# Optimization experiments

Hardware: AMD Instinct MI355X
Metric: run time of the kernel (lower is better)

## Reference

```python
import jax, jax.numpy as jnp
import numpy as np

B, T = 1, 128
R = 200000          # neurons * 4 receptor channels (output current dim)
LGN = 17400         # LGN source neurons
BKG = 100           # background source neurons
NNZ_L = 1_000_000   # lgn synapses
NNZ_B = 400_000     # bkg synapses


def setup_inputs() -> dict:
    key = jax.random.key(0)
    ks = jax.random.split(key, 8)
    lgn_spikes = (jax.random.uniform(ks[0], (B, T, LGN)) < 0.05).astype(jnp.float32)
    bkg_spikes = (jax.random.uniform(ks[1], (B, T, BKG)) < 0.1).astype(jnp.float32)
    lgn_rows = jnp.sort(jax.random.randint(ks[2], (NNZ_L,), 0, R, dtype=jnp.int32))
    lgn_cols = jax.random.randint(ks[3], (NNZ_L,), 0, LGN, dtype=jnp.int32)
    lgn_weights = jax.random.normal(ks[4], (NNZ_L,), dtype=jnp.float32) * 0.1
    bkg_rows = jnp.sort(jax.random.randint(ks[5], (NNZ_B,), 0, R, dtype=jnp.int32))
    bkg_cols = jax.random.randint(ks[6], (NNZ_B,), 0, BKG, dtype=jnp.int32)
    bkg_weights = jax.random.normal(ks[7], (NNZ_B,), dtype=jnp.float32) * 0.1
    return {
        "lgn_spikes": lgn_spikes, "bkg_spikes": bkg_spikes,
        "lgn_rows": lgn_rows, "lgn_cols": lgn_cols, "lgn_weights": lgn_weights,
        "bkg_rows": bkg_rows, "bkg_cols": bkg_cols, "bkg_weights": bkg_weights,
    }


def _sparse_current(spikes, rows, cols, weights, n_rows):
    # spikes: (B, T, C). Equivalent to transpose(sparse(R,C) @ spikes_2d^T)
    # reshaped back to (B, T, R).
    b, t, c = spikes.shape
    x2d = spikes.reshape(b * t, c)                       # (BT, C)
    vals = weights[:, None] * x2d[:, cols].T             # (nnz, BT) gathered contributions
    out = jax.ops.segment_sum(vals, rows, num_segments=n_rows)  # (R, BT)
    return out.T.reshape(b, t, n_rows)


def reference(lgn_spikes, bkg_spikes, lgn_rows, lgn_cols, lgn_weights,
              bkg_rows, bkg_cols, bkg_weights):
    lgn_current = _sparse_current(lgn_spikes, lgn_rows, lgn_cols, lgn_weights, R)
    bkg_current = _sparse_current(bkg_spikes, bkg_rows, bkg_cols, bkg_weights, R)
    return lgn_current + bkg_current
```

## Files before the change

kernel.cpp:

```cpp
#include <hip/hip_runtime.h>

#define T_STEPS 128

typedef float vfloat4 __attribute__((ext_vector_type(4)));

__global__ __launch_bounds__(256) void prep_kernel(
    const float* __restrict__ lgn_spikes, int lgn_C, uint2* __restrict__ lgn_mask,
    const float* __restrict__ bkg_spikes, int bkg_C, uint2* __restrict__ bkg_mask,
    const int* __restrict__ lgn_rows, int nnz_l, int* __restrict__ lgn_start,
    const int* __restrict__ bkg_rows, int nnz_b, int* __restrict__ bkg_start,
    int R)
{
    int gid = blockIdx.x * 256 + threadIdx.x;
    int totC = lgn_C + bkg_C;

    if (gid < totC) {
        const float* sp; uint2* mask; int C, cc;
        if (gid < lgn_C) { sp = lgn_spikes; mask = lgn_mask; C = lgn_C; cc = gid; }
        else             { sp = bkg_spikes; mask = bkg_mask; C = bkg_C; cc = gid - lgn_C; }
        unsigned int m0 = 0u, m1 = 0u, m2 = 0u, m3 = 0u;
        #pragma unroll 4
        for (int t = 0; t < 32; ++t) {
            if (sp[(size_t)(t)       * C + cc] != 0.0f) m0 |= (1u << t);
            if (sp[(size_t)(t +  32) * C + cc] != 0.0f) m1 |= (1u << t);
            if (sp[(size_t)(t +  64) * C + cc] != 0.0f) m2 |= (1u << t);
            if (sp[(size_t)(t +  96) * C + cc] != 0.0f) m3 |= (1u << t);
        }
        mask[(size_t)0 * C + cc] = make_uint2(m0, m1);
        mask[(size_t)1 * C + cc] = make_uint2(m2, m3);
        return;
    }

    int i = gid - totC;
    const int* rows; int nnz; int* start;
    if (i < nnz_l) { rows = lgn_rows; nnz = nnz_l; start = lgn_start; }
    else {
        i -= nnz_l;
        if (i >= nnz_b) return;
        rows = bkg_rows; nnz = nnz_b; start = bkg_start;
    }
    int cur  = rows[i];
    int prev = (i == 0) ? -1 : rows[i - 1];
    for (int rr = prev + 1; rr <= cur; ++rr) start[rr] = i;
    if (i == nnz - 1)
        for (int rr = cur + 1; rr <= R; ++rr) start[rr] = nnz;
}

__global__ __launch_bounds__(256, 4) void sparse_lut_kernel(
    const int* __restrict__ lgn_cols, const float* __restrict__ lgn_w,
    const int* __restrict__ lgn_start,
    const int* __restrict__ bkg_cols, const float* __restrict__ bkg_w,
    const int* __restrict__ bkg_start,
    const uint2* __restrict__ lgn_mask,
    const uint2* __restrict__ bkg_mask,
    int lgn_C, int bkg_C, int R,
    float* __restrict__ out)
{
    __shared__ float4 lut[16];
    __shared__ float tile[16 * 260];
    const int tid = threadIdx.x;
    if (tid < 16)
        lut[tid] = make_float4((float)(tid & 1), (float)((tid >> 1) & 1),
                               (float)((tid >> 2) & 1), (float)((tid >> 3) & 1));

    const int r0 = blockIdx.x * 256;
    const int r  = r0 + tid;
    const int q  = blockIdx.y;

    float acc[64];
    #pragma unroll
    for (int t = 0; t < 64; ++t) acc[t] = 0.0f;

    const uint2* lm = lgn_mask + (size_t)q * lgn_C;
    const uint2* bm = bkg_mask + (size_t)q * bkg_C;

    int l0 = 0, l1 = 0, g0 = 0, g1 = 0;
    if (r < R) {
        l0 = lgn_start[r]; l1 = lgn_start[r + 1];
        g0 = bkg_start[r]; g1 = bkg_start[r + 1];
    }
    __syncthreads();

    #define ACC_WORD(mw, base, wv)                                           \
        _Pragma("unroll")                                                    \
        for (int nb = 0; nb < 8; ++nb) {                                     \
            float4 s = lut[((mw) >> (nb * 4)) & 15u];                        \
            acc[(base) + nb * 4 + 0] = fmaf(wv, s.x, acc[(base) + nb * 4 + 0]); \
            acc[(base) + nb * 4 + 1] = fmaf(wv, s.y, acc[(base) + nb * 4 + 1]); \
            acc[(base) + nb * 4 + 2] = fmaf(wv, s.z, acc[(base) + nb * 4 + 2]); \
            acc[(base) + nb * 4 + 3] = fmaf(wv, s.w, acc[(base) + nb * 4 + 3]); \
        }

    #define ACC_RANGE(cols_a, w_a, mask_p, I0, I1)                           \
    {                                                                        \
        int i0 = (I0), i1 = (I1);                                            \
        if (i0 < i1) {                                                       \
            float w0 = w_a[i0];                                              \
            int   c1 = 0; float w1 = 0.0f;                                   \
            if (i0 + 1 < i1) { c1 = cols_a[i0 + 1]; w1 = w_a[i0 + 1]; }      \
            uint2 m0 = mask_p[cols_a[i0]];                                   \
            for (int i = i0; i < i1; ++i) {                                  \
                uint2 m1v = make_uint2(0u, 0u);                              \
                if (i + 1 < i1) m1v = mask_p[c1];                            \
                int c2 = 0; float w2 = 0.0f;                                 \
                if (i + 2 < i1) { c2 = cols_a[i + 2]; w2 = w_a[i + 2]; }     \
                ACC_WORD(m0.x, 0,  w0)                                       \
                ACC_WORD(m0.y, 32, w0)                                       \
                m0 = m1v; w0 = w1; c1 = c2; w1 = w2;                         \
            }                                                                \
        }                                                                    \
    }

    ACC_RANGE(lgn_cols, lgn_w, lm, l0, l1)
    ACC_RANGE(bkg_cols, bkg_w, bm, g0, g1)
    #undef ACC_RANGE
    #undef ACC_WORD

    const int wid  = tid >> 6;
    const int lane = tid & 63;
    #pragma unroll
    for (int pass = 0; pass < 4; ++pass) {
        #pragma unroll
        for (int p = 0; p < 16; ++p)
            tile[p * 260 + tid] = acc[pass * 16 + p];
        __syncthreads();
        #pragma unroll
        for (int pp = 0; pp < 4; ++pp) {
            int p  = wid * 4 + pp;
            int rr = r0 + 4 * lane;
            vfloat4 v = *(const vfloat4*)&tile[p * 260 + 4 * lane];
            int t = q * 64 + pass * 16 + p;
            float* dst = &out[(size_t)t * R + rr];
            if (rr + 3 < R) {
                __builtin_nontemporal_store(v, (vfloat4*)dst);
            } else {
                if (rr     < R) __builtin_nontemporal_store(v.x, dst);
                if (rr + 1 < R) __builtin_nontemporal_store(v.y, dst + 1);
                if (rr + 2 < R) __builtin_nontemporal_store(v.z, dst + 2);
            }
        }
        __syncthreads();
    }
}

__global__ __launch_bounds__(256) void sparse_fallback_kernel(
    const int* __restrict__ lgn_rows, const int* __restrict__ lgn_cols,
    const float* __restrict__ lgn_w, int nnz_l,
    const int* __restrict__ bkg_rows, const int* __restrict__ bkg_cols,
    const float* __restrict__ bkg_w, int nnz_b,
    const float* __restrict__ lgn_spikes, const float* __restrict__ bkg_spikes,
    int lgn_C, int bkg_C, int R,
    float* __restrict__ out)
{
    int r = blockIdx.x * 256 + threadIdx.x;
    int q = blockIdx.y;
    if (r >= R) return;

    float acc[32];
    #pragma unroll
    for (int t = 0; t < 32; ++t) acc[t] = 0.0f;

    {
        int lo = 0, hi = nnz_l;
        while (lo < hi) { int mid = (lo + hi) >> 1; if (lgn_rows[mid] < r) lo = mid + 1; else hi = mid; }
        for (int i = lo; i < nnz_l && lgn_rows[i] == r; ++i) {
            float wt = lgn_w[i];
            const float* sp = lgn_spikes + (size_t)(q * 32) * lgn_C + lgn_cols[i];
            #pragma unroll
            for (int t = 0; t < 32; ++t)
                acc[t] = fmaf(wt, sp[(size_t)t * lgn_C], acc[t]);
        }
    }
    {
        int lo = 0, hi = nnz_b;
        while (lo < hi) { int mid = (lo + hi) >> 1; if (bkg_rows[mid] < r) lo = mid + 1; else hi = mid; }
        for (int i = lo; i < nnz_b && bkg_rows[i] == r; ++i) {
            float wt = bkg_w[i];
            const float* sp = bkg_spikes + (size_t)(q * 32) * bkg_C + bkg_cols[i];
            #pragma unroll
            for (int t = 0; t < 32; ++t)
                acc[t] = fmaf(wt, sp[(size_t)t * bkg_C], acc[t]);
        }
    }

    float* op = out + (size_t)(q * 32) * R + r;
    #pragma unroll
    for (int t = 0; t < 32; ++t) op[(size_t)t * R] = acc[t];
}

extern "C" void kernel_launch(void* const* d_in, const int* in_sizes, int n_in,
                              void* d_out, int out_size, void* d_ws, size_t ws_size,
                              hipStream_t stream)
{
    const float* lgn_spikes = (const float*)d_in[0];
    const float* bkg_spikes = (const float*)d_in[1];
    const int*   lgn_rows   = (const int*)d_in[2];
    const int*   lgn_cols   = (const int*)d_in[3];
    const float* lgn_w      = (const float*)d_in[4];
    const int*   bkg_rows   = (const int*)d_in[5];
    const int*   bkg_cols   = (const int*)d_in[6];
    const float* bkg_w      = (const float*)d_in[7];
    float* out = (float*)d_out;

    const int nnz_l = in_sizes[2];
    const int nnz_b = in_sizes[5];
    const int lgn_C = in_sizes[0] / T_STEPS;
    const int bkg_C = in_sizes[1] / T_STEPS;
    const int R     = out_size / T_STEPS;

    size_t off = 0;
    auto take = [&](size_t bytes) { size_t o = off; off = (off + bytes + 15) & ~(size_t)15; return o; };
    size_t o_lgn_start = take((size_t)(R + 1) * sizeof(int));
    size_t o_bkg_start = take((size_t)(R + 1) * sizeof(int));
    size_t o_lgn_mask  = take((size_t)2 * lgn_C * sizeof(uint2));
    size_t o_bkg_mask  = take((size_t)2 * bkg_C * sizeof(uint2));
    size_t need = off;

    dim3 blk(256);

    if (ws_size >= need) {
        char* ws = (char*)d_ws;
        int* lgn_start = (int*)(ws + o_lgn_start);
        int* bkg_start = (int*)(ws + o_bkg_start);
        uint2* lgn_mask = (uint2*)(ws + o_lgn_mask);
        uint2* bkg_mask = (uint2*)(ws + o_bkg_mask);

        int prep_threads = (lgn_C + bkg_C) + nnz_l + nnz_b;
        prep_kernel<<<(prep_threads + 255) / 256, blk, 0, stream>>>(
            lgn_spikes, lgn_C, lgn_mask, bkg_spikes, bkg_C, bkg_mask,
            lgn_rows, nnz_l, lgn_start, bkg_rows, nnz_b, bkg_start, R);

        dim3 grid_main((R + 255) / 256, 2);
        sparse_lut_kernel<<<grid_main, blk, 0, stream>>>(
            lgn_cols, lgn_w, lgn_start,
            bkg_cols, bkg_w, bkg_start,
            lgn_mask, bkg_mask,
            lgn_C, bkg_C, R, out);
    } else {
        dim3 grid_main((R + 255) / 256, 4);
        sparse_fallback_kernel<<<grid_main, blk, 0, stream>>>(
            lgn_rows, lgn_cols, lgn_w, nnz_l,
            bkg_rows, bkg_cols, bkg_w, nnz_b,
            lgn_spikes, bkg_spikes,
            lgn_C, bkg_C, R, out);
    }
}
```

Measured before the change: 51.20 us.

## Sort rows by nnz within each block to balance warp work

Adds a kernel that bitonic-sorts the 256 rows of each block by their combined synapse count, and has the main kernel assign rows to threads through that permutation. Rows with similar work then share a wavefront, which is meant to cut divergence and idle lanes in the per-row loops. The cost is an extra kernel launch and a per-thread permutation load. Rows are also scattered, so the start loads become uncoalesced and the tile writes go through a permuted index.

```diff
diff --git a/kernel.cpp b/kernel.cpp
--- a/kernel.cpp
+++ b/kernel.cpp
@@ -46,6 +46,36 @@
         for (int rr = cur + 1; rr <= R; ++rr) start[rr] = nnz;
 }
 
+__global__ __launch_bounds__(256) void sort_rows_kernel(
+    const int* __restrict__ lgn_start, const int* __restrict__ bkg_start,
+    int R, int* __restrict__ perm)
+{
+    __shared__ unsigned int keys[256];
+    const int tid = threadIdx.x;
+    const int r   = blockIdx.x * 256 + tid;
+
+    unsigned int nnz = 0u;
+    if (r < R)
+        nnz = (unsigned int)((lgn_start[r + 1] - lgn_start[r]) +
+                             (bkg_start[r + 1] - bkg_start[r]));
+    if (nnz > 0xFFFFu) nnz = 0xFFFFu;
+    keys[tid] = (nnz << 16) | (unsigned int)tid;
+    __syncthreads();
+
+    for (int k = 2; k <= 256; k <<= 1) {
+        for (int j = k >> 1; j > 0; j >>= 1) {
+            int ixj = tid ^ j;
+            if (ixj > tid) {
+                unsigned int a = keys[tid], b = keys[ixj];
+                bool desc = (tid & k) == 0;
+                if (desc ? (a < b) : (a > b)) { keys[tid] = b; keys[ixj] = a; }
+            }
+            __syncthreads();
+        }
+    }
+    perm[blockIdx.x * 256 + tid] = (int)(keys[tid] & 0xFFFFu);
+}
+
 __global__ __launch_bounds__(256, 4) void sparse_lut_kernel(
     const int* __restrict__ lgn_cols, const float* __restrict__ lgn_w,
     const int* __restrict__ lgn_start,
@@ -53,6 +83,7 @@
     const int* __restrict__ bkg_start,
     const uint2* __restrict__ lgn_mask,
     const uint2* __restrict__ bkg_mask,
+    const int* __restrict__ perm,
     int lgn_C, int bkg_C, int R,
     float* __restrict__ out)
 {
@@ -63,9 +94,10 @@
         lut[tid] = make_float4((float)(tid & 1), (float)((tid >> 1) & 1),
                                (float)((tid >> 2) & 1), (float)((tid >> 3) & 1));
 
-    const int r0 = blockIdx.x * 256;
-    const int r  = r0 + tid;
-    const int q  = blockIdx.y;
+    const int r0  = blockIdx.x * 256;
+    const int rl  = perm[blockIdx.x * 256 + tid];
+    const int r   = r0 + rl;
+    const int q   = blockIdx.y;
 
     float acc[64];
     #pragma unroll
@@ -122,7 +154,7 @@
     for (int pass = 0; pass < 4; ++pass) {
         #pragma unroll
         for (int p = 0; p < 16; ++p)
-            tile[p * 260 + tid] = acc[pass * 16 + p];
+            tile[p * 260 + rl] = acc[pass * 16 + p];
         __syncthreads();
         #pragma unroll
         for (int pp = 0; pp < 4; ++pp) {
@@ -207,6 +239,7 @@
     const int lgn_C = in_sizes[0] / T_STEPS;
     const int bkg_C = in_sizes[1] / T_STEPS;
     const int R     = out_size / T_STEPS;
+    const int NBLK  = (R + 255) / 256;
 
     size_t off = 0;
     auto take = [&](size_t bytes) { size_t o = off; off = (off + bytes + 15) & ~(size_t)15; return o; };
@@ -214,6 +247,7 @@
     size_t o_bkg_start = take((size_t)(R + 1) * sizeof(int));
     size_t o_lgn_mask  = take((size_t)2 * lgn_C * sizeof(uint2));
     size_t o_bkg_mask  = take((size_t)2 * bkg_C * sizeof(uint2));
+    size_t o_perm      = take((size_t)NBLK * 256 * sizeof(int));
     size_t need = off;
 
     dim3 blk(256);
@@ -224,17 +258,20 @@
         int* bkg_start = (int*)(ws + o_bkg_start);
         uint2* lgn_mask = (uint2*)(ws + o_lgn_mask);
         uint2* bkg_mask = (uint2*)(ws + o_bkg_mask);
+        int* perm = (int*)(ws + o_perm);
 
         int prep_threads = (lgn_C + bkg_C) + nnz_l + nnz_b;
         prep_kernel<<<(prep_threads + 255) / 256, blk, 0, stream>>>(
             lgn_spikes, lgn_C, lgn_mask, bkg_spikes, bkg_C, bkg_mask,
             lgn_rows, nnz_l, lgn_start, bkg_rows, nnz_b, bkg_start, R);
 
-        dim3 grid_main((R + 255) / 256, 2);
+        sort_rows_kernel<<<NBLK, blk, 0, stream>>>(lgn_start, bkg_start, R, perm);
+
+        dim3 grid_main(NBLK, 2);
         sparse_lut_kernel<<<grid_main, blk, 0, stream>>>(
             lgn_cols, lgn_w, lgn_start,
             bkg_cols, bkg_w, bkg_start,
-            lgn_mask, bkg_mask,
+            lgn_mask, bkg_mask, perm,
             lgn_C, bkg_C, R, out);
     } else {
         dim3 grid_main((R + 255) / 256, 4);
```

New measurement: 60.02 us. +17.2%, slower.

## Merge LGN and background synapses into one interleaved CSR with unified mask

Applied to the files above, without the earlier changes.

Adds a merge kernel that scatters the LGN and background synapses into a single row-ordered array of packed (column, weight) pairs, with background columns offset into one unified spike-mask table. The main kernel then walks one range per row instead of two, loading one 8-byte entry per synapse instead of separate column and weight loads. This is meant to cut per-thread loop overhead and divergence from the two separate ranges, and to improve load efficiency. The cost is an extra kernel launch and a full pass that reads the original arrays and writes the merged synapse array every call.

```diff
diff --git a/kernel.cpp b/kernel.cpp
--- a/kernel.cpp
+++ b/kernel.cpp
@@ -5,8 +5,9 @@
 typedef float vfloat4 __attribute__((ext_vector_type(4)));
 
 __global__ __launch_bounds__(256) void prep_kernel(
-    const float* __restrict__ lgn_spikes, int lgn_C, uint2* __restrict__ lgn_mask,
-    const float* __restrict__ bkg_spikes, int bkg_C, uint2* __restrict__ bkg_mask,
+    const float* __restrict__ lgn_spikes, int lgn_C,
+    const float* __restrict__ bkg_spikes, int bkg_C,
+    uint2* __restrict__ mask,
     const int* __restrict__ lgn_rows, int nnz_l, int* __restrict__ lgn_start,
     const int* __restrict__ bkg_rows, int nnz_b, int* __restrict__ bkg_start,
     int R)
@@ -15,9 +16,9 @@
     int totC = lgn_C + bkg_C;
 
     if (gid < totC) {
-        const float* sp; uint2* mask; int C, cc;
-        if (gid < lgn_C) { sp = lgn_spikes; mask = lgn_mask; C = lgn_C; cc = gid; }
-        else             { sp = bkg_spikes; mask = bkg_mask; C = bkg_C; cc = gid - lgn_C; }
+        const float* sp; int C, cc;
+        if (gid < lgn_C) { sp = lgn_spikes; C = lgn_C; cc = gid; }
+        else             { sp = bkg_spikes; C = bkg_C; cc = gid - lgn_C; }
         unsigned int m0 = 0u, m1 = 0u, m2 = 0u, m3 = 0u;
         #pragma unroll 4
         for (int t = 0; t < 32; ++t) {
@@ -26,8 +27,8 @@
             if (sp[(size_t)(t +  64) * C + cc] != 0.0f) m2 |= (1u << t);
             if (sp[(size_t)(t +  96) * C + cc] != 0.0f) m3 |= (1u << t);
         }
-        mask[(size_t)0 * C + cc] = make_uint2(m0, m1);
-        mask[(size_t)1 * C + cc] = make_uint2(m2, m3);
+        mask[(size_t)0 * totC + gid] = make_uint2(m0, m1);
+        mask[(size_t)1 * totC + gid] = make_uint2(m2, m3);
         return;
     }
 
@@ -46,15 +47,35 @@
         for (int rr = cur + 1; rr <= R; ++rr) start[rr] = nnz;
 }
 
+__global__ __launch_bounds__(256) void merge_kernel(
+    const int* __restrict__ lgn_rows, const int* __restrict__ lgn_cols,
+    const float* __restrict__ lgn_w, int nnz_l,
+    const int* __restrict__ bkg_rows, const int* __restrict__ bkg_cols,
+    const float* __restrict__ bkg_w, int nnz_b,
+    const int* __restrict__ lgn_start, const int* __restrict__ bkg_start,
+    int lgn_C, uint2* __restrict__ syn)
+{
+    int gid = blockIdx.x * 256 + threadIdx.x;
+    if (gid < nnz_l) {
+        int row = lgn_rows[gid];
+        int pos = gid + bkg_start[row];
+        syn[pos] = make_uint2((unsigned int)lgn_cols[gid],
+                              __float_as_uint(lgn_w[gid]));
+    } else {
+        int j = gid - nnz_l;
+        if (j >= nnz_b) return;
+        int row = bkg_rows[j];
+        int pos = j + lgn_start[row + 1];
+        syn[pos] = make_uint2((unsigned int)(bkg_cols[j] + lgn_C),
+                              __float_as_uint(bkg_w[j]));
+    }
+}
+
 __global__ __launch_bounds__(256, 4) void sparse_lut_kernel(
-    const int* __restrict__ lgn_cols, const float* __restrict__ lgn_w,
-    const int* __restrict__ lgn_start,
-    const int* __restrict__ bkg_cols, const float* __restrict__ bkg_w,
-    const int* __restrict__ bkg_start,
-    const uint2* __restrict__ lgn_mask,
-    const uint2* __restrict__ bkg_mask,
-    int lgn_C, int bkg_C, int R,
-    float* __restrict__ out)
+    const uint2* __restrict__ syn,
+    const int* __restrict__ lgn_start, const int* __restrict__ bkg_start,
+    const uint2* __restrict__ mask,
+    int totC, int R, float* __restrict__ out)
 {
     __shared__ float4 lut[16];
     __shared__ float tile[16 * 260];
@@ -71,13 +92,12 @@
     #pragma unroll
     for (int t = 0; t < 64; ++t) acc[t] = 0.0f;
 
-    const uint2* lm = lgn_mask + (size_t)q * lgn_C;
-    const uint2* bm = bkg_mask + (size_t)q * bkg_C;
-
-    int l0 = 0, l1 = 0, g0 = 0, g1 = 0;
+    const uint2* mp = mask + (size_t)q * totC;
+
+    int m0i = 0, m1i = 0;
     if (r < R) {
-        l0 = lgn_start[r]; l1 = lgn_start[r + 1];
-        g0 = bkg_start[r]; g1 = bkg_start[r + 1];
+        m0i = lgn_start[r]     + bkg_start[r];
+        m1i = lgn_start[r + 1] + bkg_start[r + 1];
     }
     __syncthreads();
 
@@ -91,29 +111,22 @@
             acc[(base) + nb * 4 + 3] = fmaf(wv, s.w, acc[(base) + nb * 4 + 3]); \
         }
 
-    #define ACC_RANGE(cols_a, w_a, mask_p, I0, I1)                           \
-    {                                                                        \
-        int i0 = (I0), i1 = (I1);                                            \
-        if (i0 < i1) {                                                       \
-            float w0 = w_a[i0];                                              \
-            int   c1 = 0; float w1 = 0.0f;                                   \
-            if (i0 + 1 < i1) { c1 = cols_a[i0 + 1]; w1 = w_a[i0 + 1]; }      \
-            uint2 m0 = mask_p[cols_a[i0]];                                   \
-            for (int i = i0; i < i1; ++i) {                                  \
-                uint2 m1v = make_uint2(0u, 0u);                              \
-                if (i + 1 < i1) m1v = mask_p[c1];                            \
-                int c2 = 0; float w2 = 0.0f;                                 \
-                if (i + 2 < i1) { c2 = cols_a[i + 2]; w2 = w_a[i + 2]; }     \
-                ACC_WORD(m0.x, 0,  w0)                                       \
-                ACC_WORD(m0.y, 32, w0)                                       \
-                m0 = m1v; w0 = w1; c1 = c2; w1 = w2;                         \
-            }                                                                \
-        }                                                                    \
-    }
-
-    ACC_RANGE(lgn_cols, lgn_w, lm, l0, l1)
-    ACC_RANGE(bkg_cols, bkg_w, bm, g0, g1)
-    #undef ACC_RANGE
+    if (m0i < m1i) {
+        uint2 cw0 = syn[m0i];
+        uint2 cw1 = make_uint2(0u, 0u);
+        if (m0i + 1 < m1i) cw1 = syn[m0i + 1];
+        uint2 mk0 = mp[cw0.x];
+        for (int i = m0i; i < m1i; ++i) {
+            uint2 mk1 = make_uint2(0u, 0u);
+            if (i + 1 < m1i) mk1 = mp[cw1.x];
+            uint2 cw2 = make_uint2(0u, 0u);
+            if (i + 2 < m1i) cw2 = syn[i + 2];
+            float wv = __uint_as_float(cw0.y);
+            ACC_WORD(mk0.x, 0,  wv)
+            ACC_WORD(mk0.y, 32, wv)
+            mk0 = mk1; cw0 = cw1; cw1 = cw2;
+        }
+    }
     #undef ACC_WORD
 
     const int wid  = tid >> 6;
@@ -206,36 +219,41 @@
     const int nnz_b = in_sizes[5];
     const int lgn_C = in_sizes[0] / T_STEPS;
     const int bkg_C = in_sizes[1] / T_STEPS;
+    const int totC  = lgn_C + bkg_C;
     const int R     = out_size / T_STEPS;
+    const int NBLK  = (R + 255) / 256;
 
     size_t off = 0;
     auto take = [&](size_t bytes) { size_t o = off; off = (off + bytes + 15) & ~(size_t)15; return o; };
     size_t o_lgn_start = take((size_t)(R + 1) * sizeof(int));
     size_t o_bkg_start = take((size_t)(R + 1) * sizeof(int));
-    size_t o_lgn_mask  = take((size_t)2 * lgn_C * sizeof(uint2));
-    size_t o_bkg_mask  = take((size_t)2 * bkg_C * sizeof(uint2));
+    size_t o_mask      = take((size_t)2 * totC * sizeof(uint2));
+    size_t o_syn       = take((size_t)(nnz_l + nnz_b) * sizeof(uint2));
     size_t need = off;
 
     dim3 blk(256);
 
     if (ws_size >= need) {
         char* ws = (char*)d_ws;
-        int* lgn_start = (int*)(ws + o_lgn_start);
-        int* bkg_start = (int*)(ws + o_bkg_start);
-        uint2* lgn_mask = (uint2*)(ws + o_lgn_mask);
-        uint2* bkg_mask = (uint2*)(ws + o_bkg_mask);
-
-        int prep_threads = (lgn_C + bkg_C) + nnz_l + nnz_b;
+        int*   lgn_start = (int*)(ws + o_lgn_start);
+        int*   bkg_start = (int*)(ws + o_bkg_start);
+        uint2* mask      = (uint2*)(ws + o_mask);
+        uint2* syn       = (uint2*)(ws + o_syn);
+
+        int prep_threads = totC + nnz_l + nnz_b;
         prep_kernel<<<(prep_threads + 255) / 256, blk, 0, stream>>>(
-            lgn_spikes, lgn_C, lgn_mask, bkg_spikes, bkg_C, bkg_mask,
+            lgn_spikes, lgn_C, bkg_spikes, bkg_C, mask,
             lgn_rows, nnz_l, lgn_start, bkg_rows, nnz_b, bkg_start, R);
 
-        dim3 grid_main((R + 255) / 256, 2);
+        int merge_threads = nnz_l + nnz_b;
+        merge_kernel<<<(merge_threads + 255) / 256, blk, 0, stream>>>(
+            lgn_rows, lgn_cols, lgn_w, nnz_l,
+            bkg_rows, bkg_cols, bkg_w, nnz_b,
+            lgn_start, bkg_start, lgn_C, syn);
+
+        dim3 grid_main(NBLK, 2);
         sparse_lut_kernel<<<grid_main, blk, 0, stream>>>(
-            lgn_cols, lgn_w, lgn_start,
-            bkg_cols, bkg_w, bkg_start,
-            lgn_mask, bkg_mask,
-            lgn_C, bkg_C, R, out);
+            syn, lgn_start, bkg_start, mask, totC, R, out);
     } else {
         dim3 grid_main((R + 255) / 256, 4);
         sparse_fallback_kernel<<<grid_main, blk, 0, stream>>>(
```

Measured after the change: 59.20 us. 15.6% more time.
